# Optimization experiments

Hardware: AMD Instinct MI355X
Metric: run time of the kernel (lower is better)

## Reference

```python
import jax, jax.numpy as jnp
import numpy as np

DEPTH = 6
N_LEAF = 2 ** DEPTH          # 64
GATE_COUNT = N_LEAF - 1      # 63
IN_F = 512
OUT_F = 512
BATCH = 1024


def setup_inputs() -> dict:
    key = jax.random.key(0)
    k1, k2, k3 = jax.random.split(key, 3)
    x = jax.random.normal(k1, (BATCH, IN_F), dtype=jnp.float32)
    gw = jax.random.normal(k2, (IN_F, GATE_COUNT), dtype=jnp.float32)
    gb = jnp.zeros((GATE_COUNT,), dtype=jnp.float32)
    pw = jax.random.normal(k3, (OUT_F, IN_F, N_LEAF), dtype=jnp.float32)
    pb = jnp.zeros((OUT_F, N_LEAF), dtype=jnp.float32)
    return {"x": x, "gw": gw, "gb": gb, "pw": pw, "pb": pb}


def _leaf_probs(x, gw, gb, depth):
    # gatings: sigmoid(x @ gw + gb), shape [B, gate_count]
    g = jax.nn.sigmoid(x @ gw + gb)
    B = x.shape[0]
    dens = jnp.ones((B, 1), dtype=x.dtype)  # root density
    offset = 0
    for d in range(depth):
        n = 2 ** d
        gp = g[:, offset:offset + n]                    # parent gatings [B, n]
        # left child multiplies by g, right child by (1 - g), interleaved
        pair = jnp.stack([gp, 1.0 - gp], axis=-1).reshape(B, 2 * n)
        dens = jnp.repeat(dens, 2, axis=1) * pair        # [B, 2n]
        offset += n
    return dens  # [B, n_leaf]


def reference(x, gw, gb, pw, pb):
    leaf = _leaf_probs(x, gw, gb, DEPTH)                 # [B, L]
    # per-leaf linear projections, then mix with leaf probabilities
    y = jnp.einsum('bi,oil->bol', x, pw)                 # [B, O, L]
    out = jnp.einsum('bol,bl->bo', y, leaf) + leaf @ pb.T
    return out
```

## Files before the change

kernel.cpp:

```cpp
#include <hip/hip_runtime.h>
#include <hip/hip_bf16.h>

#define TDEPTH 6
#define NLEAF 64
#define NGATE 63
#define INF 512
#define OUTF 512
#define BATCH 1024
#define SPLITK 8
#define NPL 64

typedef _Float16 f16;
typedef __attribute__((ext_vector_type(2)))  f16 f16x2;
typedef __attribute__((ext_vector_type(8)))  f16 f16x8;
typedef __attribute__((ext_vector_type(4)))  float f32x4;
typedef __attribute__((ext_vector_type(16))) float f32x16;

__device__ __forceinline__ f16x8 pack8h(f32x4 a, f32x4 b) {
  f16x8 w;
  w[0] = (f16)a[0]; w[1] = (f16)a[1]; w[2] = (f16)a[2]; w[3] = (f16)a[3];
  w[4] = (f16)b[0]; w[5] = (f16)b[1]; w[6] = (f16)b[2]; w[7] = (f16)b[3];
  return w;
}

__global__ __launch_bounds__(256) void prep_kernel(
    const float* __restrict__ x, const float* __restrict__ gw,
    const float* __restrict__ gb, const float* __restrict__ pw,
    const float* __restrict__ pb, float* __restrict__ leaf,
    f16* __restrict__ pwh) {
  const int tid = threadIdx.x;
  if (blockIdx.x < 256) {
    const int wid = tid >> 6, lane = tid & 63;
    const int b = blockIdx.x * 4 + wid;
    __shared__ float g[4][NLEAF];
    if (lane < NGATE) {
      const float* xr = x + (size_t)b * INF;
      float a0 = 0.f, a1 = 0.f, a2 = 0.f, a3 = 0.f;
      #pragma unroll 4
      for (int i = 0; i < INF; i += 4) {
        a0 += xr[i + 0] * gw[(i + 0) * NGATE + lane];
        a1 += xr[i + 1] * gw[(i + 1) * NGATE + lane];
        a2 += xr[i + 2] * gw[(i + 2) * NGATE + lane];
        a3 += xr[i + 3] * gw[(i + 3) * NGATE + lane];
      }
      float t = (a0 + a1) + (a2 + a3) + gb[lane];
      g[wid][lane] = 1.0f / (1.0f + __expf(-t));
    }
    __syncthreads();
    float p = 1.0f;
    #pragma unroll
    for (int d = 0; d < TDEPTH; d++) {
      int prefix = lane >> (TDEPTH - 1 - d);
      int node = (1 << d) - 1 + (prefix >> 1);
      float gv = g[wid][node];
      p *= (prefix & 1) ? (1.0f - gv) : gv;
    }
    leaf[(size_t)b * NLEAF + lane] = p;
    return;
  }
  const unsigned Q = (blockIdx.x - 256) * 256 + tid;
  const unsigned tile = Q >> 8;
  const unsigned ot = tile / 513;
  const unsigned i = tile - ot * 513;
  const unsigned q = Q & 255;
  const unsigned r = q >> 4, p = q & 15;
  const unsigned v = p ^ r;
  const unsigned o = ot * 32 + r + 16 * (v >> 3);
  const unsigned kg = v & 7;
  const float* src = (i < INF) ? (pw + ((size_t)o * INF + i) * NLEAF + kg * 8)
                               : (pb + (size_t)o * NLEAF + kg * 8);
  f32x4 a = *(const f32x4*)src, b = *(const f32x4*)(src + 4);
  *(f16x8*)((char*)pwh + (size_t)Q * 16) = pack8h(a, b);
}

__device__ __forceinline__ void gload_lds16(const void* g, void* l) {
  __builtin_amdgcn_global_load_lds(
      (const __attribute__((address_space(1))) void*)g,
      (__attribute__((address_space(3))) void*)l, 16, 0, 0);
}

__global__ __launch_bounds__(64, 2) void gemm_kernel(
    const f16* __restrict__ pwh, const float* __restrict__ x,
    const float* __restrict__ leaf, float* __restrict__ partial) {
  __shared__ __align__(16) char Bsm[3][4096];
  __shared__ unsigned short xsm[NPL][64];

  const int lane = threadIdx.x;
  const int lo = lane & 31, half = lane >> 5;

  const int L = ((int)blockIdx.x & 7) * 256 + ((int)blockIdx.x >> 3);
  const int bt = L & 15;
  const int p = L >> 4;
  const int ot = p & 15, s = p >> 4;
  const int b0 = bt * 64;
  const int cs = s * NPL;
  const int count = NPL + (s == SPLITK - 1 ? 1 : 0);

  {
    const float* xr = x + (size_t)(b0 + lane) * INF + cs;
    #pragma unroll
    for (int c4 = 0; c4 < NPL / 4; c4++) {
      f32x4 v = *(const f32x4*)(xr + c4 * 4);
      #pragma unroll
      for (int j = 0; j < 4; j++)
        xsm[c4 * 4 + j][lane] = __builtin_bit_cast(unsigned short, (f16)v[j]);
    }
  }

  f16x8 lfb[2][4];
  #pragma unroll
  for (int mt = 0; mt < 2; mt++) {
    const float* lr = leaf + (size_t)(b0 + mt * 32 + lo) * NLEAF + half * 8;
    #pragma unroll
    for (int t4 = 0; t4 < 4; t4++)
      lfb[mt][t4] = pack8h(*(const f32x4*)(lr + t4 * 16),
                           *(const f32x4*)(lr + t4 * 16 + 4));
  }

  unsigned rdoff[4];
  {
    const unsigned r = (unsigned)(lo & 15);
    const unsigned hb = ((unsigned)(lo >> 4)) * 128 + (unsigned)half * 16;
    #pragma unroll
    for (int t4 = 0; t4 < 4; t4++)
      rdoff[t4] = r * 256 + ((hb + t4 * 32) ^ (r << 4));
  }

  const char* tb = (const char*)pwh + ((size_t)(ot * 513 + cs) << 12) +
                   (size_t)lane * 16;
  auto stage = [&](char* dstb, int t) {
    const char* srcb = tb + ((size_t)t << 12);
    #pragma unroll
    for (int j = 0; j < 4; j++)
      gload_lds16(srcb + j * 1024, dstb + j * 1024);
  };

  f32x16 acc0 = (f32x16)(0.f), acc1 = (f32x16)(0.f);

  auto do_step = [&](const char* bufc, int t) {
    unsigned pr0 = 0x3C003C00u, pr1 = 0x3C003C00u;
    if (t < NPL) {
      unsigned x0 = xsm[t][lo], x1 = xsm[t][32 + lo];
      pr0 = x0 | (x0 << 16);
      pr1 = x1 | (x1 << 16);
    }
    f16x2 v0 = __builtin_bit_cast(f16x2, pr0);
    f16x2 v1 = __builtin_bit_cast(f16x2, pr1);
    f16x8 xv80 = __builtin_shufflevector(v0, v0, 0, 1, 0, 1, 0, 1, 0, 1);
    f16x8 xv81 = __builtin_shufflevector(v1, v1, 0, 1, 0, 1, 0, 1, 0, 1);
    #pragma unroll
    for (int t4 = 0; t4 < 4; t4++) {
      f16x8 af = *(const f16x8*)(bufc + rdoff[t4]);
      f16x8 s0 = lfb[0][t4] * xv80;
      f16x8 s1 = lfb[1][t4] * xv81;
      acc0 = __builtin_amdgcn_mfma_f32_32x32x16_f16(af, s0, acc0, 0, 0, 0);
      acc1 = __builtin_amdgcn_mfma_f32_32x32x16_f16(af, s1, acc1, 0, 0, 0);
    }
  };

  char* bA = (char*)&Bsm[0][0];
  char* bB = (char*)&Bsm[1][0];
  char* bC = (char*)&Bsm[2][0];

  stage(bA, 0);
  stage(bB, 1);
  asm volatile("s_waitcnt lgkmcnt(0)" ::: "memory");

  for (int t = 0; t < count - 2; ++t) {
    stage(bC, t + 2);
    asm volatile("s_waitcnt vmcnt(8)" ::: "memory");
    do_step(bA, t);
    char* tmp = bA; bA = bB; bB = bC; bC = tmp;
  }
  asm volatile("s_waitcnt vmcnt(4)" ::: "memory");
  do_step(bA, count - 2);
  asm volatile("s_waitcnt vmcnt(0)" ::: "memory");
  do_step(bB, count - 1);

  float* dstb = partial + ((size_t)s * OUTF + ot * 32) * BATCH + b0;
  #pragma unroll
  for (int e = 0; e < 16; e++) {
    int row = (e & 3) + 8 * (e >> 2) + 4 * half;
    dstb[(size_t)row * BATCH + lo] = acc0[e];
    dstb[(size_t)row * BATCH + 32 + lo] = acc1[e];
  }
}

__global__ __launch_bounds__(256) void reduce_kernel(
    const float* __restrict__ partial, float* __restrict__ out) {
  __shared__ float tile[32][65];
  const int t = threadIdx.x;
  const int O0 = ((int)blockIdx.x >> 4) * 32;
  const int B0 = ((int)blockIdx.x & 15) * 64;
  #pragma unroll
  for (int rep = 0; rep < 8; rep++) {
    const int idx = rep * 256 + t;
    const int o = idx >> 6, b = idx & 63;
    float sum = 0.f;
    #pragma unroll
    for (int s = 0; s < SPLITK; s++)
      sum += partial[((size_t)s * OUTF + O0 + o) * BATCH + B0 + b];
    tile[o][b] = sum;
  }
  __syncthreads();
  #pragma unroll
  for (int rep = 0; rep < 8; rep++) {
    const int idx = rep * 256 + t;
    const int b = idx >> 5, o = idx & 31;
    out[(size_t)(B0 + b) * OUTF + O0 + o] = tile[o][b];
  }
}

extern "C" void kernel_launch(void* const* d_in, const int* in_sizes, int n_in,
                              void* d_out, int out_size, void* d_ws, size_t ws_size,
                              hipStream_t stream) {
  const float* x  = (const float*)d_in[0];
  const float* gw = (const float*)d_in[1];
  const float* gb = (const float*)d_in[2];
  const float* pw = (const float*)d_in[3];
  const float* pb = (const float*)d_in[4];
  float* out = (float*)d_out;

  float* leaf    = (float*)d_ws;
  f16*   pwh     = (f16*)((char*)d_ws + (256 << 10));
  float* partial = (float*)((char*)d_ws + (256 << 10) + (size_t)16 * 513 * 4096);

  prep_kernel<<<256 + 8208, 256, 0, stream>>>(x, gw, gb, pw, pb, leaf, pwh);
  gemm_kernel<<<2048, 64, 0, stream>>>(pwh, x, leaf, partial);
  reduce_kernel<<<256, 256, 0, stream>>>(partial, out);
}
```

Baseline: 72.14 us.

## Coalesce weight-prep reads and double split-K with register-held x operands

The prep kernel now walks pw contiguously, 16 chunks per thread, and scatters the swizzled fp16 tiles on write, instead of reading pw strided per output tile; the bias tiles go to a separate block. The GEMM moves from SPLITK 8 to 16 with half as many K steps per block and keeps packed x values in registers instead of LDS. It drops from triple to double buffering with explicit sched_barriers and raises the launch-bounds occupancy hint to 4. The aim is better DRAM efficiency on the large weight conversion and more concurrent waves in the GEMM, at the cost of twice the partial-sum traffic for the reduce kernel.

```diff
diff --git a/kernel.cpp b/kernel.cpp
--- a/kernel.cpp
+++ b/kernel.cpp
@@ -7,8 +7,8 @@
 #define INF 512
 #define OUTF 512
 #define BATCH 1024
-#define SPLITK 8
-#define NPL 64
+#define SPLITK 16
+#define NPL 32
 
 typedef _Float16 f16;
 typedef __attribute__((ext_vector_type(2)))  f16 f16x2;
@@ -58,19 +58,35 @@
     leaf[(size_t)b * NLEAF + lane] = p;
     return;
   }
-  const unsigned Q = (blockIdx.x - 256) * 256 + tid;
-  const unsigned tile = Q >> 8;
-  const unsigned ot = tile / 513;
-  const unsigned i = tile - ot * 513;
-  const unsigned q = Q & 255;
-  const unsigned r = q >> 4, p = q & 15;
-  const unsigned v = p ^ r;
-  const unsigned o = ot * 32 + r + 16 * (v >> 3);
-  const unsigned kg = v & 7;
-  const float* src = (i < INF) ? (pw + ((size_t)o * INF + i) * NLEAF + kg * 8)
-                               : (pb + (size_t)o * NLEAF + kg * 8);
-  f32x4 a = *(const f32x4*)src, b = *(const f32x4*)(src + 4);
-  *(f16x8*)((char*)pwh + (size_t)Q * 16) = pack8h(a, b);
+  if (blockIdx.x < 768) {
+    const unsigned base = (blockIdx.x - 256) * 4096;
+    #pragma unroll
+    for (int rep = 0; rep < 16; rep++) {
+      const unsigned T = base + rep * 256 + tid;
+      const unsigned o = T >> 12, rem = T & 4095;
+      const unsigned i = rem >> 3, kg = rem & 7;
+      const float* src = pw + (size_t)T * 8;
+      f32x4 a = *(const f32x4*)src, b = *(const f32x4*)(src + 4);
+      const unsigned r = o & 15;
+      const unsigned p = ((((o >> 4) & 1) << 3) | kg) ^ r;
+      char* dst = (char*)pwh + (((size_t)((o >> 5) * 513 + i)) << 12) +
+                  r * 256 + p * 16;
+      *(f16x8*)dst = pack8h(a, b);
+    }
+  } else {
+    #pragma unroll
+    for (int rep = 0; rep < 16; rep++) {
+      const unsigned T = rep * 256 + tid;
+      const unsigned o = T >> 3, kg = T & 7;
+      const float* src = pb + (size_t)T * 8;
+      f32x4 a = *(const f32x4*)src, b = *(const f32x4*)(src + 4);
+      const unsigned r = o & 15;
+      const unsigned p = ((((o >> 4) & 1) << 3) | kg) ^ r;
+      char* dst = (char*)pwh + (((size_t)((o >> 5) * 513 + 512)) << 12) +
+                  r * 256 + p * 16;
+      *(f16x8*)dst = pack8h(a, b);
+    }
+  }
 }
 
 __device__ __forceinline__ void gload_lds16(const void* g, void* l) {
@@ -79,31 +95,35 @@
       (__attribute__((address_space(3))) void*)l, 16, 0, 0);
 }
 
-__global__ __launch_bounds__(64, 2) void gemm_kernel(
+__global__ __launch_bounds__(64, 4) void gemm_kernel(
     const f16* __restrict__ pwh, const float* __restrict__ x,
     const float* __restrict__ leaf, float* __restrict__ partial) {
-  __shared__ __align__(16) char Bsm[3][4096];
-  __shared__ unsigned short xsm[NPL][64];
+  __shared__ __align__(16) char Bsm[2][4096];
 
   const int lane = threadIdx.x;
   const int lo = lane & 31, half = lane >> 5;
 
-  const int L = ((int)blockIdx.x & 7) * 256 + ((int)blockIdx.x >> 3);
-  const int bt = L & 15;
-  const int p = L >> 4;
-  const int ot = p & 15, s = p >> 4;
+  const int L = ((int)blockIdx.x & 7) * 512 + ((int)blockIdx.x >> 3);
+  const int s = L >> 8;
+  const int rem = L & 255;
+  const int ot = rem >> 4, bt = rem & 15;
   const int b0 = bt * 64;
   const int cs = s * NPL;
-  const int count = NPL + (s == SPLITK - 1 ? 1 : 0);
-
+
+  unsigned xu[NPL];
   {
-    const float* xr = x + (size_t)(b0 + lane) * INF + cs;
+    const float* x0 = x + (size_t)(b0 + lo) * INF + cs;
+    const float* x1 = x + (size_t)(b0 + 32 + lo) * INF + cs;
     #pragma unroll
     for (int c4 = 0; c4 < NPL / 4; c4++) {
-      f32x4 v = *(const f32x4*)(xr + c4 * 4);
+      f32x4 a = *(const f32x4*)(x0 + c4 * 4);
+      f32x4 b = *(const f32x4*)(x1 + c4 * 4);
       #pragma unroll
-      for (int j = 0; j < 4; j++)
-        xsm[c4 * 4 + j][lane] = __builtin_bit_cast(unsigned short, (f16)v[j]);
+      for (int j = 0; j < 4; j++) {
+        unsigned la = (unsigned)__builtin_bit_cast(unsigned short, (f16)a[j]);
+        unsigned lb = (unsigned)__builtin_bit_cast(unsigned short, (f16)b[j]);
+        xu[c4 * 4 + j] = la | (lb << 16);
+      }
     }
   }
 
@@ -128,6 +148,10 @@
 
   const char* tb = (const char*)pwh + ((size_t)(ot * 513 + cs) << 12) +
                    (size_t)lane * 16;
+  char* bufs[2] = {(char*)&Bsm[0][0], (char*)&Bsm[1][0]};
+
+  f32x16 acc0 = (f32x16)(0.f), acc1 = (f32x16)(0.f);
+
   auto stage = [&](char* dstb, int t) {
     const char* srcb = tb + ((size_t)t << 12);
     #pragma unroll
@@ -135,15 +159,7 @@
       gload_lds16(srcb + j * 1024, dstb + j * 1024);
   };
 
-  f32x16 acc0 = (f32x16)(0.f), acc1 = (f32x16)(0.f);
-
-  auto do_step = [&](const char* bufc, int t) {
-    unsigned pr0 = 0x3C003C00u, pr1 = 0x3C003C00u;
-    if (t < NPL) {
-      unsigned x0 = xsm[t][lo], x1 = xsm[t][32 + lo];
-      pr0 = x0 | (x0 << 16);
-      pr1 = x1 | (x1 << 16);
-    }
+  auto mfma_step = [&](const char* bufc, unsigned pr0, unsigned pr1) {
     f16x2 v0 = __builtin_bit_cast(f16x2, pr0);
     f16x2 v1 = __builtin_bit_cast(f16x2, pr1);
     f16x8 xv80 = __builtin_shufflevector(v0, v0, 0, 1, 0, 1, 0, 1, 0, 1);
@@ -158,24 +174,29 @@
     }
   };
 
-  char* bA = (char*)&Bsm[0][0];
-  char* bB = (char*)&Bsm[1][0];
-  char* bC = (char*)&Bsm[2][0];
-
-  stage(bA, 0);
-  stage(bB, 1);
-  asm volatile("s_waitcnt lgkmcnt(0)" ::: "memory");
-
-  for (int t = 0; t < count - 2; ++t) {
-    stage(bC, t + 2);
-    asm volatile("s_waitcnt vmcnt(8)" ::: "memory");
-    do_step(bA, t);
-    char* tmp = bA; bA = bB; bB = bC; bC = tmp;
-  }
-  asm volatile("s_waitcnt vmcnt(4)" ::: "memory");
-  do_step(bA, count - 2);
-  asm volatile("s_waitcnt vmcnt(0)" ::: "memory");
-  do_step(bB, count - 1);
+  stage(bufs[0], 0);
+
+  #pragma unroll
+  for (int t = 0; t < NPL; t++) {
+    __builtin_amdgcn_sched_barrier(0);
+    asm volatile("s_waitcnt lgkmcnt(0)" ::: "memory");
+    __builtin_amdgcn_sched_barrier(0);
+    stage(bufs[(t + 1) & 1], t + 1);
+    __builtin_amdgcn_sched_barrier(0);
+    asm volatile("s_waitcnt vmcnt(4)" ::: "memory");
+    __builtin_amdgcn_sched_barrier(0);
+    const unsigned u = xu[t];
+    unsigned p0 = u & 0xffffu;  p0 |= (p0 << 16);
+    unsigned p1 = u >> 16;      p1 |= (p1 << 16);
+    mfma_step(bufs[t & 1], p0, p1);
+  }
+
+  if (s == SPLITK - 1) {
+    __builtin_amdgcn_sched_barrier(0);
+    asm volatile("s_waitcnt vmcnt(0)" ::: "memory");
+    __builtin_amdgcn_sched_barrier(0);
+    mfma_step(bufs[0], 0x3C003C00u, 0x3C003C00u);
+  }
 
   float* dstb = partial + ((size_t)s * OUTF + ot * 32) * BATCH + b0;
   #pragma unroll
@@ -225,7 +246,7 @@
   f16*   pwh     = (f16*)((char*)d_ws + (256 << 10));
   float* partial = (float*)((char*)d_ws + (256 << 10) + (size_t)16 * 513 * 4096);
 
-  prep_kernel<<<256 + 8208, 256, 0, stream>>>(x, gw, gb, pw, pb, leaf, pwh);
-  gemm_kernel<<<2048, 64, 0, stream>>>(pwh, x, leaf, partial);
+  prep_kernel<<<769, 256, 0, stream>>>(x, gw, gb, pw, pb, leaf, pwh);
+  gemm_kernel<<<4096, 64, 0, stream>>>(pwh, x, leaf, partial);
   reduce_kernel<<<256, 256, 0, stream>>>(partial, out);
 }
```

Result: slower. 82.25 us (+14.0%).
